# Kernel tuning notes

Measured on AMD Instinct MI355X. Metric: run time of the kernel, lower is better.

The kernel has to match this reference:

```python
import jax, jax.numpy as jnp
import numpy as np
from jax import lax

EPS = 1e-08


def setup_inputs() -> dict:
    key = jax.random.key(0)
    k1, k2, k3, k4 = jax.random.split(key, 4)
    b, cin, cout, hw, kk = 32, 256, 256, 64, 3
    fan_in = cin * kk * kk
    # kaiming_normal_(a=0, mode='fan_in', nonlinearity='leaky_relu') -> gain=sqrt(2), std=sqrt(2/fan_in)
    w_std = np.sqrt(2.0 / fan_in).astype(np.float32)
    return {
        "x": jax.random.normal(k1, (b, cin, hw, hw), dtype=jnp.float32),
        "y": jax.random.normal(k2, (b, cin), dtype=jnp.float32),
        "weight": jax.random.normal(k3, (cout, cin, kk, kk), dtype=jnp.float32) * w_std,
        "bias": jax.random.normal(k4, (cout,), dtype=jnp.float32) * 0.1,
    }


def _modulated_conv(x, y, weight, bias):
    # x: [b, cin, h, w]; y: [b, cin]; weight: [cout, cin, kh, kw]; bias: [cout]
    # modulate: per-sample scale of input channels
    w = weight[None] * (y[:, None, :, None, None] + 1.0)  # [b, cout, cin, kh, kw]
    # demodulate: normalize each (sample, out-channel) filter
    d = lax.rsqrt(jnp.sum(w * w, axis=(2, 3, 4), keepdims=True) + EPS)
    w = w * d

    def conv_one(xi, wi):
        # xi: [cin, h, w]; wi: [cout, cin, kh, kw]
        out = lax.conv_general_dilated(
            xi[None], wi, window_strides=(1, 1), padding="SAME",
            dimension_numbers=("NCHW", "OIHW", "NCHW"))
        return out[0]  # [cout, h, w]

    out = jax.vmap(conv_one)(x, w)  # [b, cout, h, w]
    return out + bias[None, :, None, None]


def reference(x, y, weight, bias):
    return _modulated_conv(x, y, weight, bias)
```

## Files before the change

### kernel.cpp

```cpp
#include <hip/hip_runtime.h>
#include <hip/hip_bf16.h>

typedef __attribute__((ext_vector_type(8))) short short8;
typedef __attribute__((ext_vector_type(4))) float f32x4;

#define XT_IMG_BYTES (66*66*256*2)
#define XT_TOTAL_BYTES (32*XT_IMG_BYTES)
#define WM_ROW_BYTES (2304*2)
#define WM_IMG_BYTES (256*WM_ROW_BYTES)

static __device__ __forceinline__ void async16(void* lds, const void* g) {
  __builtin_amdgcn_global_load_lds((const __attribute__((address_space(1))) void*)g,
                                   (__attribute__((address_space(3))) void*)lds, 16, 0, 0);
}
static __device__ __forceinline__ ushort f2bf(float f) {
  __hip_bfloat16 h = __float2bfloat16(f);
  return *reinterpret_cast<ushort*>(&h);
}

__global__ __launch_bounds__(256) void k_zeroborder(uint4* __restrict__ xT4) {
  const int b = blockIdx.x;
  const int t = threadIdx.x;
  const uint4 z = make_uint4(0u, 0u, 0u, 0u);
  uint4* base = xT4 + (size_t)b * (66 * 66 * 32);
  uint4* r0  = base;
  uint4* r65 = base + (size_t)65 * 66 * 32;
  for (int i = t; i < 2112; i += 256) { r0[i] = z; r65[i] = z; }
  for (int i = t; i < 2048; i += 256) {
    int r = (i >> 5) + 1, c = i & 31;
    base[((size_t)r * 66 + 0)  * 32 + c] = z;
    base[((size_t)r * 66 + 65) * 32 + c] = z;
  }
}

__global__ __launch_bounds__(256) void k_xpose(const float* __restrict__ x,
                                               ushort* __restrict__ xT) {
  __shared__ float lds[64][65];
  const int bx = blockIdx.x;
  const int b  = bx >> 8;
  const int h  = (bx >> 2) & 63;
  const int c0 = (bx & 3) << 6;
  const int t  = threadIdx.x;
  const int tw = t & 63, tg = t >> 6;
  const float* xp = x + (size_t)(b * 256 + c0) * 4096 + h * 64 + tw;
#pragma unroll
  for (int j = 0; j < 16; ++j) {
    int il = j * 4 + tg;
    lds[il][tw] = xp[(size_t)il * 4096];
  }
  __syncthreads();
  const int q  = t & 15;
  const int w0 = t >> 4;
  ushort* op = xT + (size_t)b * (66 * 66 * 256) + ((size_t)(h + 1) * 66 + 1) * 256 + c0;
#pragma unroll
  for (int j = 0; j < 4; ++j) {
    const int wl = j * 16 + w0;
    ushort4 v;
    v.x = f2bf(lds[4 * q + 0][wl]);
    v.y = f2bf(lds[4 * q + 1][wl]);
    v.z = f2bf(lds[4 * q + 2][wl]);
    v.w = f2bf(lds[4 * q + 3][wl]);
    *(ushort4*)(op + (size_t)wl * 256 + 4 * q) = v;
  }
}

__global__ __launch_bounds__(256) void k_modw(const float* __restrict__ W,
                                              const float* __restrict__ y,
                                              ushort* __restrict__ wmod) {
  __shared__ float red[256];
  const int b = blockIdx.x >> 8, o = blockIdx.x & 255, t = threadIdx.x;
  const float* wp = W + (size_t)(o * 256 + t) * 9;
  float wr[9];
#pragma unroll
  for (int r = 0; r < 9; ++r) wr[r] = wp[r];
  const float ym = y[b * 256 + t] + 1.0f;
  float ss = 0.f;
#pragma unroll
  for (int r = 0; r < 9; ++r) ss += wr[r] * wr[r];
  red[t] = ss * ym * ym;
  __syncthreads();
  for (int s = 128; s > 0; s >>= 1) {
    if (t < s) red[t] += red[t + s];
    __syncthreads();
  }
  const float sc = rsqrtf(red[0] + 1e-8f) * ym;
  ushort* op = wmod + (size_t)(b * 256 + o) * 2304 + t;
#pragma unroll
  for (int r = 0; r < 9; ++r) op[r * 256] = f2bf(wr[r] * sc);
}

__global__ __launch_bounds__(256, 2) void k_gemm(const ushort* __restrict__ wmod,
                                                 const ushort* __restrict__ xT,
                                                 const float* __restrict__ bias,
                                                 float* __restrict__ out) {
  __shared__ ushort ldsA[128 * 32];
  __shared__ ushort ldsB[128 * 32];
  const int t = threadIdx.x;
  const int bx = blockIdx.x;
  const int xcd = bx & 7;
  const int idx = bx >> 3;
  const int b   = xcd + ((idx >> 6) << 3);
  const int rem = idx & 63;
  const int o0 = (rem & 1) << 7;
  const int tn = rem >> 1;
  const int n0 = tn << 7;
  const int h0 = tn << 1;
  const int l = t & 63, w = t >> 6;
  const int ln = l & 15, kq = l >> 4;
  const int wm = w >> 1, wn = w & 1;

  const char* gA = (const char*)wmod + (size_t)b * WM_IMG_BYTES +
                   (size_t)(o0 + (t >> 2)) * WM_ROW_BYTES + (t & 3) * 16;
  const char* xTb = (const char*)xT + (size_t)b * XT_IMG_BYTES + (t & 3) * 16;
  const int wl = (t >> 2) & 63;

  f32x4 acc[4][4];
  const f32x4 z4 = {0.f, 0.f, 0.f, 0.f};
#pragma unroll
  for (int i = 0; i < 4; ++i)
#pragma unroll
    for (int j = 0; j < 4; ++j) acc[i][j] = z4;

  ushort* lA = ldsA + t * 8;
  ushort* lB = ldsB + t * 8;
  const ushort* rA = ldsA + (wm * 64 + ln) * 32 + kq * 8;
  const ushort* rB = ldsB + (wn * 64 + ln) * 32 + kq * 8;

#pragma unroll 1
  for (int r = 0; r < 9; ++r) {
    const int kh = r / 3, kw = r % 3;
    const char* gB = xTb + (((h0 + kh) * 66 + wl + kw) * 512);
#pragma unroll 1
    for (int s = 0; s < 8; ++s) {
      async16(lA, gA);
      async16(lA + 2048, gA + 64 * WM_ROW_BYTES);
      async16(lB, gB);
      async16(lB + 2048, gB + 66 * 512);
      asm volatile("s_waitcnt vmcnt(0)" ::: "memory");
      __syncthreads();
      short8 af[4], bf[4];
#pragma unroll
      for (int mi = 0; mi < 4; ++mi) af[mi] = *(const short8*)(rA + mi * 16 * 32);
#pragma unroll
      for (int ni = 0; ni < 4; ++ni) bf[ni] = *(const short8*)(rB + ni * 16 * 32);
#pragma unroll
      for (int mi = 0; mi < 4; ++mi)
#pragma unroll
        for (int ni = 0; ni < 4; ++ni)
          acc[mi][ni] = __builtin_amdgcn_mfma_f32_16x16x32_bf16(af[mi], bf[ni], acc[mi][ni], 0, 0, 0);
      __syncthreads();
      gA += 64;
      gB += 64;
    }
  }

  float* outB = out + (size_t)(b * 256 + o0 + wm * 64) * 4096 + n0 + wn * 64 + ln;
#pragma unroll
  for (int mi = 0; mi < 4; ++mi) {
#pragma unroll
    for (int rg = 0; rg < 4; ++rg) {
      const int orow = mi * 16 + kq * 4 + rg;
      const float bv = bias[o0 + wm * 64 + orow];
      float* po = outB + (size_t)orow * 4096;
#pragma unroll
      for (int ni = 0; ni < 4; ++ni) po[ni * 16] = acc[mi][ni][rg] + bv;
    }
  }
}

extern "C" void kernel_launch(void* const* d_in, const int* in_sizes, int n_in,
                              void* d_out, int out_size, void* d_ws, size_t ws_size,
                              hipStream_t stream) {
  const float* x    = (const float*)d_in[0];
  const float* y    = (const float*)d_in[1];
  const float* W    = (const float*)d_in[2];
  const float* bias = (const float*)d_in[3];
  float* out = (float*)d_out;

  ushort* xT   = (ushort*)d_ws;
  ushort* wmod = (ushort*)((char*)d_ws + (size_t)XT_TOTAL_BYTES);

  k_zeroborder<<<32,          256, 0, stream>>>((uint4*)d_ws);
  k_xpose     <<<32 * 64 * 4, 256, 0, stream>>>(x, xT);
  k_modw      <<<32 * 256,    256, 0, stream>>>(W, y, wmod);
  k_gemm      <<<32 * 64,     256, 0, stream>>>(wmod, xT, bias, out);
}
```

Before: 419.9 us.

## Move modulation onto input and demodulation into epilogue, sharing one weight

Each sample no longer gets its own modulated bf16 weight tensor. The per-channel scale (y+1) is folded into the input during the transpose, and the demodulation factor is applied to the accumulator in the GEMM epilogue. One shared bf16 weight and a small per-(b,o) scale table are precomputed. This removes writing and reading 32 per-sample weight copies, so the GEMM's A operand becomes shared and cache-resident. The transpose kernel now handles four rows per block. Rounding to bf16 now happens after scaling x rather than after scaling w.

```diff
diff --git a/kernel.cpp b/kernel.cpp
--- a/kernel.cpp
+++ b/kernel.cpp
@@ -6,8 +6,11 @@
 
 #define XT_IMG_BYTES (66*66*256*2)
 #define XT_TOTAL_BYTES (32*XT_IMG_BYTES)
-#define WM_ROW_BYTES (2304*2)
-#define WM_IMG_BYTES (256*WM_ROW_BYTES)
+#define WB_ROW_BYTES (2304*2)
+#define WB_OFF   (XT_TOTAL_BYTES)
+#define W2T_OFF  (WB_OFF + 256*WB_ROW_BYTES)
+#define SC_OFF   (W2T_OFF + 256*256*4)
+#define YM_OFF   (SC_OFF  + 32*256*4)
 
 static __device__ __forceinline__ void async16(void* lds, const void* g) {
   __builtin_amdgcn_global_load_lds((const __attribute__((address_space(1))) void*)g,
@@ -33,64 +36,76 @@
   }
 }
 
+__global__ __launch_bounds__(256) void k_wprep(const float* __restrict__ W,
+                                               ushort* __restrict__ Wb,
+                                               float* __restrict__ W2T) {
+  const int o = blockIdx.x, i = threadIdx.x;
+  const float* wp = W + (size_t)(o * 256 + i) * 9;
+  float wr[9], ss = 0.f;
+#pragma unroll
+  for (int r = 0; r < 9; ++r) { wr[r] = wp[r]; ss += wr[r] * wr[r]; }
+  W2T[i * 256 + o] = ss;
+  ushort* op = Wb + (size_t)o * 2304 + i;
+#pragma unroll
+  for (int r = 0; r < 9; ++r) op[r * 256] = f2bf(wr[r]);
+}
+
+__global__ __launch_bounds__(256) void k_scale(const float* __restrict__ y,
+                                               const float* __restrict__ W2T,
+                                               float* __restrict__ sc,
+                                               float* __restrict__ ymod) {
+  __shared__ float ym2[256];
+  const int b = blockIdx.x, t = threadIdx.x;
+  const float ym = y[b * 256 + t] + 1.0f;
+  ymod[b * 256 + t] = ym;
+  ym2[t] = ym * ym;
+  __syncthreads();
+  float acc = 0.f;
+#pragma unroll 8
+  for (int i = 0; i < 256; ++i) acc += W2T[i * 256 + t] * ym2[i];
+  sc[b * 256 + t] = rsqrtf(acc + 1e-8f);
+}
+
 __global__ __launch_bounds__(256) void k_xpose(const float* __restrict__ x,
+                                               const float* __restrict__ ymod,
                                                ushort* __restrict__ xT) {
   __shared__ float lds[64][65];
+  __shared__ float ym_s[64];
   const int bx = blockIdx.x;
-  const int b  = bx >> 8;
-  const int h  = (bx >> 2) & 63;
+  const int b  = bx >> 6;
+  const int hg = (bx >> 2) & 15;
   const int c0 = (bx & 3) << 6;
   const int t  = threadIdx.x;
+  if (t < 64) ym_s[t] = ymod[b * 256 + c0 + t];
   const int tw = t & 63, tg = t >> 6;
-  const float* xp = x + (size_t)(b * 256 + c0) * 4096 + h * 64 + tw;
-#pragma unroll
-  for (int j = 0; j < 16; ++j) {
-    int il = j * 4 + tg;
-    lds[il][tw] = xp[(size_t)il * 4096];
-  }
-  __syncthreads();
-  const int q  = t & 15;
-  const int w0 = t >> 4;
-  ushort* op = xT + (size_t)b * (66 * 66 * 256) + ((size_t)(h + 1) * 66 + 1) * 256 + c0;
-#pragma unroll
-  for (int j = 0; j < 4; ++j) {
-    const int wl = j * 16 + w0;
-    ushort4 v;
-    v.x = f2bf(lds[4 * q + 0][wl]);
-    v.y = f2bf(lds[4 * q + 1][wl]);
-    v.z = f2bf(lds[4 * q + 2][wl]);
-    v.w = f2bf(lds[4 * q + 3][wl]);
-    *(ushort4*)(op + (size_t)wl * 256 + 4 * q) = v;
-  }
-}
-
-__global__ __launch_bounds__(256) void k_modw(const float* __restrict__ W,
-                                              const float* __restrict__ y,
-                                              ushort* __restrict__ wmod) {
-  __shared__ float red[256];
-  const int b = blockIdx.x >> 8, o = blockIdx.x & 255, t = threadIdx.x;
-  const float* wp = W + (size_t)(o * 256 + t) * 9;
-  float wr[9];
-#pragma unroll
-  for (int r = 0; r < 9; ++r) wr[r] = wp[r];
-  const float ym = y[b * 256 + t] + 1.0f;
-  float ss = 0.f;
-#pragma unroll
-  for (int r = 0; r < 9; ++r) ss += wr[r] * wr[r];
-  red[t] = ss * ym * ym;
-  __syncthreads();
-  for (int s = 128; s > 0; s >>= 1) {
-    if (t < s) red[t] += red[t + s];
+  const int q  = t & 15, w0 = t >> 4;
+  for (int hh = 0; hh < 4; ++hh) {
+    const int h = hg * 4 + hh;
     __syncthreads();
-  }
-  const float sc = rsqrtf(red[0] + 1e-8f) * ym;
-  ushort* op = wmod + (size_t)(b * 256 + o) * 2304 + t;
-#pragma unroll
-  for (int r = 0; r < 9; ++r) op[r * 256] = f2bf(wr[r] * sc);
-}
-
-__global__ __launch_bounds__(256, 2) void k_gemm(const ushort* __restrict__ wmod,
+    const float* xp = x + (size_t)(b * 256 + c0) * 4096 + h * 64 + tw;
+#pragma unroll
+    for (int j = 0; j < 16; ++j) {
+      int il = j * 4 + tg;
+      lds[il][tw] = xp[(size_t)il * 4096];
+    }
+    __syncthreads();
+    ushort* op = xT + (size_t)b * (66 * 66 * 256) + ((size_t)(h + 1) * 66 + 1) * 256 + c0;
+#pragma unroll
+    for (int j = 0; j < 4; ++j) {
+      const int wl = j * 16 + w0;
+      ushort4 v;
+      v.x = f2bf(lds[4 * q + 0][wl] * ym_s[4 * q + 0]);
+      v.y = f2bf(lds[4 * q + 1][wl] * ym_s[4 * q + 1]);
+      v.z = f2bf(lds[4 * q + 2][wl] * ym_s[4 * q + 2]);
+      v.w = f2bf(lds[4 * q + 3][wl] * ym_s[4 * q + 3]);
+      *(ushort4*)(op + (size_t)wl * 256 + 4 * q) = v;
+    }
+  }
+}
+
+__global__ __launch_bounds__(256, 2) void k_gemm(const ushort* __restrict__ Wb,
                                                  const ushort* __restrict__ xT,
+                                                 const float* __restrict__ sc,
                                                  const float* __restrict__ bias,
                                                  float* __restrict__ out) {
   __shared__ ushort ldsA[128 * 32];
@@ -109,8 +124,7 @@
   const int ln = l & 15, kq = l >> 4;
   const int wm = w >> 1, wn = w & 1;
 
-  const char* gA = (const char*)wmod + (size_t)b * WM_IMG_BYTES +
-                   (size_t)(o0 + (t >> 2)) * WM_ROW_BYTES + (t & 3) * 16;
+  const char* gA = (const char*)Wb + (size_t)(o0 + (t >> 2)) * WB_ROW_BYTES + (t & 3) * 16;
   const char* xTb = (const char*)xT + (size_t)b * XT_IMG_BYTES + (t & 3) * 16;
   const int wl = (t >> 2) & 63;
 
@@ -133,7 +147,7 @@
 #pragma unroll 1
     for (int s = 0; s < 8; ++s) {
       async16(lA, gA);
-      async16(lA + 2048, gA + 64 * WM_ROW_BYTES);
+      async16(lA + 2048, gA + 64 * WB_ROW_BYTES);
       async16(lB, gB);
       async16(lB + 2048, gB + 66 * 512);
       asm volatile("s_waitcnt vmcnt(0)" ::: "memory");
@@ -155,15 +169,17 @@
   }
 
   float* outB = out + (size_t)(b * 256 + o0 + wm * 64) * 4096 + n0 + wn * 64 + ln;
+  const float* scB = sc + b * 256 + o0 + wm * 64;
 #pragma unroll
   for (int mi = 0; mi < 4; ++mi) {
 #pragma unroll
     for (int rg = 0; rg < 4; ++rg) {
       const int orow = mi * 16 + kq * 4 + rg;
+      const float scv = scB[orow];
       const float bv = bias[o0 + wm * 64 + orow];
       float* po = outB + (size_t)orow * 4096;
 #pragma unroll
-      for (int ni = 0; ni < 4; ++ni) po[ni * 16] = acc[mi][ni][rg] + bv;
+      for (int ni = 0; ni < 4; ++ni) po[ni * 16] = acc[mi][ni][rg] * scv + bv;
     }
   }
 }
@@ -177,11 +193,16 @@
   const float* bias = (const float*)d_in[3];
   float* out = (float*)d_out;
 
-  ushort* xT   = (ushort*)d_ws;
-  ushort* wmod = (ushort*)((char*)d_ws + (size_t)XT_TOTAL_BYTES);
-
-  k_zeroborder<<<32,          256, 0, stream>>>((uint4*)d_ws);
-  k_xpose     <<<32 * 64 * 4, 256, 0, stream>>>(x, xT);
-  k_modw      <<<32 * 256,    256, 0, stream>>>(W, y, wmod);
-  k_gemm      <<<32 * 64,     256, 0, stream>>>(wmod, xT, bias, out);
-}
+  char* ws = (char*)d_ws;
+  ushort* xT   = (ushort*)ws;
+  ushort* Wb   = (ushort*)(ws + WB_OFF);
+  float*  W2T  = (float*) (ws + W2T_OFF);
+  float*  sc   = (float*) (ws + SC_OFF);
+  float*  ymod = (float*) (ws + YM_OFF);
+
+  k_zeroborder<<<32,       256, 0, stream>>>((uint4*)d_ws);
+  k_wprep     <<<256,      256, 0, stream>>>(W, Wb, W2T);
+  k_scale     <<<32,       256, 0, stream>>>(y, W2T, sc, ymod);
+  k_xpose     <<<32 * 64,  256, 0, stream>>>(x, ymod, xT);
+  k_gemm      <<<32 * 64,  256, 0, stream>>>(Wb, xT, sc, bias, out);
+}
```

Measured after the change: 425.6 us. No clear change (+1.4%).
